# Performance work log

Hardware: AMD Instinct MI355X
Metric: run time of the kernel (lower is better)

Reference implementation:

```python
import jax, jax.numpy as jnp
import numpy as np

N_NODES = 50000
N_EDGES = 800000
LEAKY_SLOPE = 0.01
DROPOUT_P = 0.5


def _graph_conv(src, dst, x, W, b):
    """DGL GraphConv with norm='both': D_out^{-1/2} A D_in^{-1/2} X W + b."""
    n = x.shape[0]
    ones = jnp.ones((src.shape[0],), dtype=x.dtype)
    deg_out = jax.ops.segment_sum(ones, src, num_segments=n)  # out-degree of src nodes
    deg_in = jax.ops.segment_sum(ones, dst, num_segments=n)   # in-degree of dst nodes
    norm_src = jax.lax.rsqrt(jnp.maximum(deg_out, 1.0))
    norm_dst = jax.lax.rsqrt(jnp.maximum(deg_in, 1.0))
    h = (x * norm_src[:, None]) @ W          # apply weight before aggregation
    agg = jax.ops.segment_sum(h[src], dst, num_segments=n)  # SpMM aggregate
    return agg * norm_dst[:, None] + b


def _dropout(x, key, p=DROPOUT_P):
    keep = jax.random.bernoulli(key, 1.0 - p, x.shape)
    return jnp.where(keep, x / (1.0 - p), jnp.zeros((), x.dtype))


def setup_inputs() -> dict:
    key = jax.random.key(0)
    ks = jax.random.split(key, 8)
    features = jax.random.normal(ks[0], (N_NODES, 128), dtype=jnp.float32)
    src = jax.random.randint(ks[1], (N_EDGES,), 0, N_NODES, dtype=jnp.int64)
    dst = jax.random.randint(ks[2], (N_EDGES,), 0, N_NODES, dtype=jnp.int64)
    s1 = 1.0 / np.sqrt(128.0)
    s3 = 1.0 / np.sqrt(128.0)
    W1 = jax.random.normal(ks[3], (128, 128), dtype=jnp.float32) * s1
    W2 = jax.random.normal(ks[4], (128, 128), dtype=jnp.float32) * s1
    W3 = jax.random.normal(ks[5], (128, 64), dtype=jnp.float32) * s3
    b1 = jnp.zeros((128,), dtype=jnp.float32)
    b2 = jnp.zeros((128,), dtype=jnp.float32)
    b3 = jnp.zeros((64,), dtype=jnp.float32)
    return {"features": features, "src": src, "dst": dst,
            "W1": W1, "b1": b1, "W2": W2, "b2": b2, "W3": W3, "b3": b3}


def reference(features, src, dst, W1, b1, W2, b2, W3, b3):
    dk = jax.random.split(jax.random.key(42), 3)
    h = jax.nn.leaky_relu(_graph_conv(src, dst, features, W1, b1), LEAKY_SLOPE)
    h = _dropout(h, dk[0])
    h = jax.nn.leaky_relu(_graph_conv(src, dst, h, W2, b2), LEAKY_SLOPE)
    h = _dropout(h, dk[1])
    h = jax.nn.leaky_relu(_graph_conv(src, dst, h, W3, b3), LEAKY_SLOPE)
    h = _dropout(h, dk[2])
    return h
```

## Files before the change

### kernel.cpp

```cpp
#include <hip/hip_runtime.h>
#include <hip/hip_fp16.h>
#include <stdint.h>

using half8 = __attribute__((ext_vector_type(8))) _Float16;
using f32x4 = __attribute__((ext_vector_type(4))) float;

#define SLOT_CAP 64
#define LDW 136
#define NBINS 50176
#define LWORDS 12544
#define NCHUNK 128

#define TFR(r) { x0 += x1; x1 = (x1 << r) | (x1 >> (32 - r)); x1 ^= x0; }

__host__ __device__ inline void threefry2x32(uint32_t k0, uint32_t k1,
                                             uint32_t c0, uint32_t c1,
                                             uint32_t& o0, uint32_t& o1) {
  uint32_t ks2 = k0 ^ k1 ^ 0x1BD11BDAu;
  uint32_t x0 = c0 + k0, x1 = c1 + k1;
  TFR(13) TFR(15) TFR(26) TFR(6)  x0 += k1;  x1 += ks2 + 1u;
  TFR(17) TFR(29) TFR(16) TFR(24) x0 += ks2; x1 += k0 + 2u;
  TFR(13) TFR(15) TFR(26) TFR(6)  x0 += k0;  x1 += k1 + 3u;
  TFR(17) TFR(29) TFR(16) TFR(24) x0 += k1;  x1 += ks2 + 4u;
  TFR(13) TFR(15) TFR(26) TFR(6)  x0 += ks2; x1 += k0 + 5u;
  o0 = x0; o1 = x1;
}

__device__ inline float tf_uniform(uint32_t k0, uint32_t k1, uint32_t i) {
  uint32_t o0, o1;
  threefry2x32(k0, k1, 0u, i, o0, o1);
  uint32_t bits = o0 ^ o1;
  return __uint_as_float((bits >> 9) | 0x3F800000u) - 1.0f;
}

__device__ __host__ inline uint16_t f2h_bits_host(float f) {
  _Float16 h = (_Float16)f;
  union { _Float16 h; uint16_t u; } c; c.h = h; return c.u;
}
__device__ inline uint16_t f2h(float f) {
  union { _Float16 h; uint16_t u; } c; c.h = (_Float16)f; return c.u;
}
__device__ inline uint32_t pack2h(float a, float b) {
  return (uint32_t)f2h(a) | ((uint32_t)f2h(b) << 16);
}
__device__ inline __half2 u2h2(uint32_t u) {
  union { uint32_t u; __half2 h; } c; c.u = u; return c.h;
}

__device__ inline void hacc(__half2* a, uint4 r) {
  a[0] = __hadd2(a[0], u2h2(r.x));
  a[1] = __hadd2(a[1], u2h2(r.y));
  a[2] = __hadd2(a[2], u2h2(r.z));
  a[3] = __hadd2(a[3], u2h2(r.w));
}

__global__ __launch_bounds__(256) void build_hist_kernel(
    const int* __restrict__ src, const int* __restrict__ dst,
    uint16_t* __restrict__ histD, uint16_t* __restrict__ histS,
    const float* __restrict__ W1, const float* __restrict__ W2,
    const float* __restrict__ W3, uint16_t* __restrict__ Wt,
    int n, int nE, int HR, int EPB) {
  const int bid = (int)blockIdx.x;
  if (bid >= 512) {
    int i = (bid - 512) * 256 + (int)threadIdx.x;
    float v;
    if (i < 16384) {
      int nr = i >> 7, k = i & 127;
      v = W1[k * 128 + nr];
    } else if (i < 32768) {
      int j = i - 16384, nr = j >> 7, k = j & 127;
      v = W2[k * 128 + nr];
    } else if (i < 40960) {
      int j = i - 32768, nr = j >> 7, k = j & 127;
      v = W3[k * 64 + nr];
    } else return;
    Wt[i] = f2h(v);
    return;
  }

  __shared__ uint32_t bins[LWORDS];
  const bool isSrc = bid >= 256;
  const int c = bid & 127;
  const int h = (bid >> 7) & 1;
  const int lo = h * HR;
  const int* keys = isSrc ? src : dst;
  uint16_t* hist = isSrc ? histS : histD;

  for (int i = threadIdx.x; i < LWORDS; i += 256) bins[i] = 0u;
  __syncthreads();

  const int e0 = c * EPB, e1 = min(e0 + EPB, nE);
  for (int e = e0 + (int)threadIdx.x; e < e1; e += 256) {
    int k = keys[e] - lo;
    if ((unsigned)k < (unsigned)HR)
      atomicAdd(&bins[k >> 1], 1u << ((k & 1) * 16));
  }
  __syncthreads();

  uint32_t* out = (uint32_t*)(hist + (size_t)c * NBINS + lo);
  const int wlim = (min(HR, n - lo) + 1) >> 1;
  for (int i = threadIdx.x; i < wlim; i += 256) out[i] = bins[i];
}

__global__ __launch_bounds__(256) void reduce_kernel(
    uint16_t* __restrict__ histD, const uint16_t* __restrict__ histS,
    int* __restrict__ degin, float* __restrict__ nsrc, int n) {
  const int v = blockIdx.x * 256 + (int)threadIdx.x;
  if (v >= n) return;
  uint32_t run = 0;
  #pragma unroll 4
  for (int c = 0; c < NCHUNK; ++c) {
    size_t idx = (size_t)c * NBINS + v;
    uint16_t x = histD[idx];
    histD[idx] = (uint16_t)run;
    run += x;
  }
  degin[v] = (int)run;
  uint32_t s = 0;
  #pragma unroll 4
  for (int c = 0; c < NCHUNK; ++c) s += histS[(size_t)c * NBINS + v];
  nsrc[v] = rsqrtf(fmaxf((float)s, 1.0f));
}

__global__ __launch_bounds__(256) void scatter_gemm1_kernel(
    const int* __restrict__ src, const int* __restrict__ dst,
    const uint16_t* __restrict__ cumD, uint16_t* __restrict__ edge_slots,
    const float* __restrict__ X, const float* __restrict__ nsrc,
    const uint16_t* __restrict__ Wt1, uint16_t* __restrict__ h1,
    int n, int nE, int HR, int EPB) {
  __shared__ uint32_t bins[LWORDS];
  const int bid = (int)blockIdx.x;

  if (bid < 256) {
    const int c = bid & 127;
    const int h = (bid >> 7) & 1;
    const int lo = h * HR;

    for (int i = threadIdx.x; i < LWORDS; i += 256) bins[i] = 0u;
    __syncthreads();

    const int e0 = c * EPB, e1 = min(e0 + EPB, nE);
    for (int e = e0 + (int)threadIdx.x; e < e1; e += 256) {
      int d = dst[e];
      int k = d - lo;
      if ((unsigned)k < (unsigned)HR) {
        uint32_t old = atomicAdd(&bins[k >> 1], 1u << ((k & 1) * 16));
        int rank = (int)((old >> ((k & 1) * 16)) & 0xFFFFu);
        int pos = (int)cumD[(size_t)c * NBINS + d] + rank;
        if (pos < SLOT_CAP) edge_slots[((size_t)d << 6) + pos] = (uint16_t)src[e];
      }
    }
    return;
  }

  const int r0 = (bid - 256) * 64;
  const int tid = (int)threadIdx.x;
  const int wave = tid >> 6, lane = tid & 63;
  const int wm = wave & 1, wn = wave >> 1;
  const int lane15 = lane & 15, quad = lane >> 4;

  const int rowA0 = r0 + wm * 32 + lane15;
  const int rowA1 = rowA0 + 16;
  const bool v0 = rowA0 < n, v1 = rowA1 < n;

  f32x4 acc[2][4] = {};
  #pragma unroll
  for (int kc = 0; kc < 128; kc += 32) {
    const int ko = kc + quad * 8;
    half8 a0 = {}, a1 = {};
    if (v0) {
      float4 x0 = *(const float4*)&X[(size_t)rowA0 * 128 + ko];
      float4 x1 = *(const float4*)&X[(size_t)rowA0 * 128 + ko + 4];
      a0[0] = (_Float16)x0.x; a0[1] = (_Float16)x0.y;
      a0[2] = (_Float16)x0.z; a0[3] = (_Float16)x0.w;
      a0[4] = (_Float16)x1.x; a0[5] = (_Float16)x1.y;
      a0[6] = (_Float16)x1.z; a0[7] = (_Float16)x1.w;
    }
    if (v1) {
      float4 x0 = *(const float4*)&X[(size_t)rowA1 * 128 + ko];
      float4 x1 = *(const float4*)&X[(size_t)rowA1 * 128 + ko + 4];
      a1[0] = (_Float16)x0.x; a1[1] = (_Float16)x0.y;
      a1[2] = (_Float16)x0.z; a1[3] = (_Float16)x0.w;
      a1[4] = (_Float16)x1.x; a1[5] = (_Float16)x1.y;
      a1[6] = (_Float16)x1.z; a1[7] = (_Float16)x1.w;
    }
    #pragma unroll
    for (int nt = 0; nt < 4; ++nt) {
      int nn = wn * 64 + nt * 16 + lane15;
      half8 b = *(const half8*)&Wt1[nn * 128 + ko];
      acc[0][nt] = __builtin_amdgcn_mfma_f32_16x16x32_f16(a0, b, acc[0][nt], 0, 0, 0);
      acc[1][nt] = __builtin_amdgcn_mfma_f32_16x16x32_f16(a1, b, acc[1][nt], 0, 0, 0);
    }
  }

  #pragma unroll
  for (int mt = 0; mt < 2; ++mt) {
    #pragma unroll
    for (int reg = 0; reg < 4; ++reg) {
      int row = r0 + wm * 32 + mt * 16 + quad * 4 + reg;
      if (row < n) {
        float nsr = nsrc[row];
        #pragma unroll
        for (int nt = 0; nt < 4; ++nt) {
          int col = wn * 64 + nt * 16 + lane15;
          h1[(size_t)row * 128 + col] = f2h(acc[mt][nt][reg] * nsr);
        }
      }
    }
  }
}

template<int NCOLS>
__global__ __launch_bounds__(256) void fuse_gather_gemm_kernel(
    const uint16_t* __restrict__ h_in, const int* __restrict__ degin,
    const uint16_t* __restrict__ edge_slots, const float* __restrict__ nsrc,
    const float* __restrict__ bias, const uint16_t* __restrict__ Wt,
    uint16_t* __restrict__ h_out, uint32_t k0, uint32_t k1, int n) {
  __shared__ uint16_t Xs[32 * LDW];
  __shared__ float ns_s[32];
  const int r0 = (int)blockIdx.x * 32;
  const int tid = (int)threadIdx.x;

  if (tid < 32) {
    int row = r0 + tid;
    ns_s[tid] = (row < n) ? nsrc[row] : 1.0f;
  }

  const int nl = tid >> 3;
  const int node = r0 + nl;
  const int c16 = (tid & 7) * 16;

  if (node < n) {
    __half2 ha[8];
    #pragma unroll
    for (int j = 0; j < 8; ++j) ha[j] = __half2(__float2half(0.f), __float2half(0.f));

    const int dgi = degin[node];
    const int deg = min(dgi, SLOT_CAP);
    const uint16_t* slots = edge_slots + ((size_t)node << 6);
    const uint16_t* hb = h_in + c16;

    int e = 0;
    for (; e + 8 <= deg; e += 8) {
      uint4 sl = *(const uint4*)&slots[e];
      const uint16_t* p0 = hb + ((size_t)(sl.x & 0xFFFF) << 7);
      const uint16_t* p1 = hb + ((size_t)(sl.x >> 16) << 7);
      const uint16_t* p2 = hb + ((size_t)(sl.y & 0xFFFF) << 7);
      const uint16_t* p3 = hb + ((size_t)(sl.y >> 16) << 7);
      const uint16_t* p4 = hb + ((size_t)(sl.z & 0xFFFF) << 7);
      const uint16_t* p5 = hb + ((size_t)(sl.z >> 16) << 7);
      const uint16_t* p6 = hb + ((size_t)(sl.w & 0xFFFF) << 7);
      const uint16_t* p7 = hb + ((size_t)(sl.w >> 16) << 7);
      uint4 a0 = *(const uint4*)p0, b0 = *(const uint4*)(p0 + 8);
      uint4 a1 = *(const uint4*)p1, b1 = *(const uint4*)(p1 + 8);
      uint4 a2 = *(const uint4*)p2, b2 = *(const uint4*)(p2 + 8);
      uint4 a3 = *(const uint4*)p3, b3 = *(const uint4*)(p3 + 8);
      uint4 a4 = *(const uint4*)p4, b4 = *(const uint4*)(p4 + 8);
      uint4 a5 = *(const uint4*)p5, b5 = *(const uint4*)(p5 + 8);
      uint4 a6 = *(const uint4*)p6, b6 = *(const uint4*)(p6 + 8);
      uint4 a7 = *(const uint4*)p7, b7 = *(const uint4*)(p7 + 8);
      hacc(ha, a0); hacc(ha + 4, b0); hacc(ha, a1); hacc(ha + 4, b1);
      hacc(ha, a2); hacc(ha + 4, b2); hacc(ha, a3); hacc(ha + 4, b3);
      hacc(ha, a4); hacc(ha + 4, b4); hacc(ha, a5); hacc(ha + 4, b5);
      hacc(ha, a6); hacc(ha + 4, b6); hacc(ha, a7); hacc(ha + 4, b7);
    }
    for (; e < deg; ++e) {
      const uint16_t* pr = hb + ((size_t)slots[e] << 7);
      uint4 ra = *(const uint4*)pr, rb = *(const uint4*)(pr + 8);
      hacc(ha, ra); hacc(ha + 4, rb);
    }

    float acc[16];
    #pragma unroll
    for (int j = 0; j < 8; ++j) {
      float2 f = __half22float2(ha[j]);
      acc[2 * j] = f.x; acc[2 * j + 1] = f.y;
    }

    const float nd = rsqrtf(fmaxf((float)dgi, 1.0f));
    const float4 b0 = *(const float4*)&bias[c16];
    const float4 b1 = *(const float4*)&bias[c16 + 4];
    const float4 b2 = *(const float4*)&bias[c16 + 8];
    const float4 b3 = *(const float4*)&bias[c16 + 12];
    const float bb[16] = {b0.x, b0.y, b0.z, b0.w, b1.x, b1.y, b1.z, b1.w,
                          b2.x, b2.y, b2.z, b2.w, b3.x, b3.y, b3.z, b3.w};
    const uint32_t i0 = (uint32_t)(node * 128 + c16);

    float o[16];
    #pragma unroll
    for (int j = 0; j < 16; ++j) {
      float v = acc[j] * nd + bb[j];
      v = (v >= 0.f) ? v : 0.01f * v;
      o[j] = (tf_uniform(k0, k1, i0 + (uint32_t)j) < 0.5f) ? v * 2.0f : 0.0f;
    }

    uint4 w0, w1;
    w0.x = pack2h(o[0], o[1]);   w0.y = pack2h(o[2], o[3]);
    w0.z = pack2h(o[4], o[5]);   w0.w = pack2h(o[6], o[7]);
    w1.x = pack2h(o[8], o[9]);   w1.y = pack2h(o[10], o[11]);
    w1.z = pack2h(o[12], o[13]); w1.w = pack2h(o[14], o[15]);
    *(uint4*)&Xs[nl * LDW + c16] = w0;
    *(uint4*)&Xs[nl * LDW + c16 + 8] = w1;
  } else {
    uint4 z = make_uint4(0u, 0u, 0u, 0u);
    *(uint4*)&Xs[nl * LDW + c16] = z;
    *(uint4*)&Xs[nl * LDW + c16 + 8] = z;
  }
  __syncthreads();

  const int wave = tid >> 6, lane = tid & 63;
  const int wm = wave & 1, wn = wave >> 1;
  const int lane15 = lane & 15, quad = lane >> 4;
  constexpr int NT = NCOLS / 32;

  f32x4 acc[NT] = {};
  #pragma unroll
  for (int kc = 0; kc < 128; kc += 32) {
    const int ko = kc + quad * 8;
    half8 a = *(const half8*)&Xs[(wm * 16 + lane15) * LDW + ko];
    #pragma unroll
    for (int nt = 0; nt < NT; ++nt) {
      int nn = wn * (NCOLS / 2) + nt * 16 + lane15;
      half8 b = *(const half8*)&Wt[nn * 128 + ko];
      acc[nt] = __builtin_amdgcn_mfma_f32_16x16x32_f16(a, b, acc[nt], 0, 0, 0);
    }
  }

  #pragma unroll
  for (int nt = 0; nt < NT; ++nt) {
    #pragma unroll
    for (int reg = 0; reg < 4; ++reg) {
      int rl = wm * 16 + quad * 4 + reg;
      int row = r0 + rl;
      if (row < n) {
        int col = wn * (NCOLS / 2) + nt * 16 + lane15;
        h_out[(size_t)row * NCOLS + col] = f2h(acc[nt][reg] * ns_s[rl]);
      }
    }
  }
}

__global__ __launch_bounds__(256) void gather_out_kernel(
    const uint16_t* __restrict__ h3, const int* __restrict__ degin,
    const uint16_t* __restrict__ edge_slots, const float* __restrict__ bias,
    float* __restrict__ out, uint32_t k0, uint32_t k1, int n) {
  const int node = (int)blockIdx.x * 32 + (int)(threadIdx.x >> 3);
  if (node >= n) return;
  const int c8 = (threadIdx.x & 7) * 8;

  const int dgi = degin[node];
  const int deg = min(dgi, SLOT_CAP);
  const uint16_t* slots = edge_slots + ((size_t)node << 6);
  const uint16_t* hb = h3 + c8;

  __half2 ha[4];
  #pragma unroll
  for (int j = 0; j < 4; ++j) ha[j] = __half2(__float2half(0.f), __float2half(0.f));

  int e = 0;
  for (; e + 8 <= deg; e += 8) {
    uint4 sl = *(const uint4*)&slots[e];
    uint4 r0 = *(const uint4*)(hb + ((size_t)(sl.x & 0xFFFF) << 6));
    uint4 r1 = *(const uint4*)(hb + ((size_t)(sl.x >> 16) << 6));
    uint4 r2 = *(const uint4*)(hb + ((size_t)(sl.y & 0xFFFF) << 6));
    uint4 r3 = *(const uint4*)(hb + ((size_t)(sl.y >> 16) << 6));
    uint4 r4 = *(const uint4*)(hb + ((size_t)(sl.z & 0xFFFF) << 6));
    uint4 r5 = *(const uint4*)(hb + ((size_t)(sl.z >> 16) << 6));
    uint4 r6 = *(const uint4*)(hb + ((size_t)(sl.w & 0xFFFF) << 6));
    uint4 r7 = *(const uint4*)(hb + ((size_t)(sl.w >> 16) << 6));
    hacc(ha, r0); hacc(ha, r1); hacc(ha, r2); hacc(ha, r3);
    hacc(ha, r4); hacc(ha, r5); hacc(ha, r6); hacc(ha, r7);
  }
  for (; e < deg; ++e) {
    uint4 r = *(const uint4*)(hb + ((size_t)slots[e] << 6));
    hacc(ha, r);
  }

  float acc[8];
  #pragma unroll
  for (int j = 0; j < 4; ++j) {
    float2 f = __half22float2(ha[j]);
    acc[2 * j] = f.x; acc[2 * j + 1] = f.y;
  }

  const float nd = rsqrtf(fmaxf((float)dgi, 1.0f));
  const float4 b0 = *(const float4*)&bias[c8];
  const float4 b1 = *(const float4*)&bias[c8 + 4];
  const float bb[8] = {b0.x, b0.y, b0.z, b0.w, b1.x, b1.y, b1.z, b1.w};
  const uint32_t i0 = (uint32_t)(node * 64 + c8);

  float o[8];
  #pragma unroll
  for (int j = 0; j < 8; ++j) {
    float v = acc[j] * nd + bb[j];
    v = (v >= 0.f) ? v : 0.01f * v;
    o[j] = (tf_uniform(k0, k1, i0 + (uint32_t)j) < 0.5f) ? v * 2.0f : 0.0f;
  }

  float* op = &out[(size_t)node * 64 + c8];
  *(float4*)op = make_float4(o[0], o[1], o[2], o[3]);
  *(float4*)(op + 4) = make_float4(o[4], o[5], o[6], o[7]);
}

extern "C" void kernel_launch(void* const* d_in, const int* in_sizes, int n_in,
                              void* d_out, int out_size, void* d_ws, size_t ws_size,
                              hipStream_t stream) {
  const float* features = (const float*)d_in[0];
  const int*   src      = (const int*)d_in[1];
  const int*   dst      = (const int*)d_in[2];
  const float* W1       = (const float*)d_in[3];
  const float* b1       = (const float*)d_in[4];
  const float* W2       = (const float*)d_in[5];
  const float* b2       = (const float*)d_in[6];
  const float* W3       = (const float*)d_in[7];
  const float* b3       = (const float*)d_in[8];
  float* out = (float*)d_out;

  const int n  = in_sizes[0] / 128;
  const int nE = in_sizes[1];

  char* p = (char*)d_ws;
  uint16_t* histD      = (uint16_t*)p; p += (size_t)NCHUNK * NBINS * 2;
  uint16_t* histS      = (uint16_t*)p; p += (size_t)NCHUNK * NBINS * 2;
  int* degin           = (int*)p;      p += (size_t)n * 4;
  float* nsrc          = (float*)p;    p += (size_t)n * 4;
  uint16_t* edge_slots = (uint16_t*)p; p += (size_t)n * SLOT_CAP * 2;
  uint16_t* Wt         = (uint16_t*)p; p += 40960 * 2;
  uint16_t* h1         = (uint16_t*)p; p += (size_t)n * 128 * 2;
  uint16_t* h2         = (uint16_t*)p; p += (size_t)n * 128 * 2;
  uint16_t* h3         = (uint16_t*)p;

  uint32_t dk[3][2];
  for (uint32_t i = 0; i < 3; ++i)
    threefry2x32(0u, 42u, 0u, i, dk[i][0], dk[i][1]);

  const int EPB = (nE + NCHUNK - 1) / NCHUNK;
  int HR = ((n + 3) / 2) & ~1;
  if (HR > 2 * LWORDS) HR = 2 * LWORDS;
  const int gb64 = (n + 63) / 64;
  const int gb32 = (n + 31) / 32;

  build_hist_kernel<<<672, 256, 0, stream>>>(src, dst, histD, histS,
                                             W1, W2, W3, Wt, n, nE, HR, EPB);
  reduce_kernel<<<(n + 255) / 256, 256, 0, stream>>>(histD, histS, degin, nsrc, n);
  scatter_gemm1_kernel<<<256 + gb64, 256, 0, stream>>>(
      src, dst, histD, edge_slots, features, nsrc, Wt, h1, n, nE, HR, EPB);
  fuse_gather_gemm_kernel<128><<<gb32, 256, 0, stream>>>(
      h1, degin, edge_slots, nsrc, b1, Wt + 16384, h2, dk[0][0], dk[0][1], n);
  fuse_gather_gemm_kernel<64><<<gb32, 256, 0, stream>>>(
      h2, degin, edge_slots, nsrc, b2, Wt + 32768, h3, dk[1][0], dk[1][1], n);
  gather_out_kernel<<<(n + 31) / 32, 256, 0, stream>>>(
      h3, degin, edge_slots, b3, out, dk[2][0], dk[2][1], n);
}
```

Baseline: 262.6 us.

## Software-pipeline neighbor gathers with padded slot lists pointing to a zero row

After: 248.7 us. -5.3%, faster.

```diff
diff --git a/kernel.cpp b/kernel.cpp
--- a/kernel.cpp
+++ b/kernel.cpp
@@ -33,10 +33,6 @@
   return __uint_as_float((bits >> 9) | 0x3F800000u) - 1.0f;
 }
 
-__device__ __host__ inline uint16_t f2h_bits_host(float f) {
-  _Float16 h = (_Float16)f;
-  union { _Float16 h; uint16_t u; } c; c.h = h; return c.u;
-}
 __device__ inline uint16_t f2h(float f) {
   union { _Float16 h; uint16_t u; } c; c.h = (_Float16)f; return c.u;
 }
@@ -54,13 +50,79 @@
   a[3] = __hadd2(a[3], u2h2(r.w));
 }
 
+#define GDECL \
+  uint4 A0, A1, A2, A3, A4, A5, A6, A7, B0, B1, B2, B3, B4, B5, B6, B7, \
+        C0, C1, C2, C3, C4, C5, C6, C7, D0, D1, D2, D3, D4, D5, D6, D7;
+
+#define GPTRS(sl, P) \
+  const uint16_t* P##0 = hb + ((size_t)((sl).x & 0xFFFFu) << 7); \
+  const uint16_t* P##1 = hb + ((size_t)((sl).x >> 16) << 7);     \
+  const uint16_t* P##2 = hb + ((size_t)((sl).y & 0xFFFFu) << 7); \
+  const uint16_t* P##3 = hb + ((size_t)((sl).y >> 16) << 7);     \
+  const uint16_t* P##4 = hb + ((size_t)((sl).z & 0xFFFFu) << 7); \
+  const uint16_t* P##5 = hb + ((size_t)((sl).z >> 16) << 7);     \
+  const uint16_t* P##6 = hb + ((size_t)((sl).w & 0xFFFFu) << 7); \
+  const uint16_t* P##7 = hb + ((size_t)((sl).w >> 16) << 7);
+
+#define GLOAD(P, X, Y) \
+  X##0 = *(const uint4*)P##0; Y##0 = *(const uint4*)(P##0 + 8); \
+  X##1 = *(const uint4*)P##1; Y##1 = *(const uint4*)(P##1 + 8); \
+  X##2 = *(const uint4*)P##2; Y##2 = *(const uint4*)(P##2 + 8); \
+  X##3 = *(const uint4*)P##3; Y##3 = *(const uint4*)(P##3 + 8); \
+  X##4 = *(const uint4*)P##4; Y##4 = *(const uint4*)(P##4 + 8); \
+  X##5 = *(const uint4*)P##5; Y##5 = *(const uint4*)(P##5 + 8); \
+  X##6 = *(const uint4*)P##6; Y##6 = *(const uint4*)(P##6 + 8); \
+  X##7 = *(const uint4*)P##7; Y##7 = *(const uint4*)(P##7 + 8);
+
+#define GHACC(X, Y) \
+  hacc(ha, X##0); hacc(ha + 4, Y##0); \
+  hacc(ha, X##1); hacc(ha + 4, Y##1); \
+  hacc(ha, X##2); hacc(ha + 4, Y##2); \
+  hacc(ha, X##3); hacc(ha + 4, Y##3); \
+  hacc(ha, X##4); hacc(ha + 4, Y##4); \
+  hacc(ha, X##5); hacc(ha + 4, Y##5); \
+  hacc(ha, X##6); hacc(ha + 4, Y##6); \
+  hacc(ha, X##7); hacc(ha + 4, Y##7);
+
+#define ODECL uint4 A0, A1, A2, A3, A4, A5, A6, A7, C0, C1, C2, C3, C4, C5, C6, C7;
+
+#define OPTRS(sl, P) \
+  const uint16_t* P##0 = hb + ((size_t)((sl).x & 0xFFFFu) << 6); \
+  const uint16_t* P##1 = hb + ((size_t)((sl).x >> 16) << 6);     \
+  const uint16_t* P##2 = hb + ((size_t)((sl).y & 0xFFFFu) << 6); \
+  const uint16_t* P##3 = hb + ((size_t)((sl).y >> 16) << 6);     \
+  const uint16_t* P##4 = hb + ((size_t)((sl).z & 0xFFFFu) << 6); \
+  const uint16_t* P##5 = hb + ((size_t)((sl).z >> 16) << 6);     \
+  const uint16_t* P##6 = hb + ((size_t)((sl).w & 0xFFFFu) << 6); \
+  const uint16_t* P##7 = hb + ((size_t)((sl).w >> 16) << 6);
+
+#define OLOAD(P, X) \
+  X##0 = *(const uint4*)P##0; X##1 = *(const uint4*)P##1; \
+  X##2 = *(const uint4*)P##2; X##3 = *(const uint4*)P##3; \
+  X##4 = *(const uint4*)P##4; X##5 = *(const uint4*)P##5; \
+  X##6 = *(const uint4*)P##6; X##7 = *(const uint4*)P##7;
+
+#define OHACC(X) \
+  hacc(ha, X##0); hacc(ha, X##1); hacc(ha, X##2); hacc(ha, X##3); \
+  hacc(ha, X##4); hacc(ha, X##5); hacc(ha, X##6); hacc(ha, X##7);
+
 __global__ __launch_bounds__(256) void build_hist_kernel(
     const int* __restrict__ src, const int* __restrict__ dst,
     uint16_t* __restrict__ histD, uint16_t* __restrict__ histS,
     const float* __restrict__ W1, const float* __restrict__ W2,
     const float* __restrict__ W3, uint16_t* __restrict__ Wt,
+    uint16_t* __restrict__ edge_slots,
     int n, int nE, int HR, int EPB) {
   const int bid = (int)blockIdx.x;
+  if (bid >= 672) {
+    const uint32_t pk = ((uint32_t)n << 16) | (uint32_t)(n & 0xFFFF);
+    uint4 f; f.x = pk; f.y = pk; f.z = pk; f.w = pk;
+    uint4* es4 = (uint4*)edge_slots;
+    const int total = n * (SLOT_CAP / 8);
+    for (int i = (bid - 672) * 256 + (int)threadIdx.x; i < total; i += 256 * 256)
+      es4[i] = f;
+    return;
+  }
   if (bid >= 512) {
     int i = (bid - 512) * 256 + (int)threadIdx.x;
     float v;
@@ -198,20 +260,18 @@
     #pragma unroll
     for (int reg = 0; reg < 4; ++reg) {
       int row = r0 + wm * 32 + mt * 16 + quad * 4 + reg;
-      if (row < n) {
-        float nsr = nsrc[row];
-        #pragma unroll
-        for (int nt = 0; nt < 4; ++nt) {
-          int col = wn * 64 + nt * 16 + lane15;
-          h1[(size_t)row * 128 + col] = f2h(acc[mt][nt][reg] * nsr);
-        }
+      float nsr = (row < n) ? nsrc[row] : 0.0f;
+      #pragma unroll
+      for (int nt = 0; nt < 4; ++nt) {
+        int col = wn * 64 + nt * 16 + lane15;
+        h1[(size_t)row * 128 + col] = f2h(acc[mt][nt][reg] * nsr);
       }
     }
   }
 }
 
 template<int NCOLS>
-__global__ __launch_bounds__(256) void fuse_gather_gemm_kernel(
+__global__ __launch_bounds__(256, 3) void fuse_gather_gemm_kernel(
     const uint16_t* __restrict__ h_in, const int* __restrict__ degin,
     const uint16_t* __restrict__ edge_slots, const float* __restrict__ nsrc,
     const float* __restrict__ bias, const uint16_t* __restrict__ Wt,
@@ -239,35 +299,33 @@
     const int deg = min(dgi, SLOT_CAP);
     const uint16_t* slots = edge_slots + ((size_t)node << 6);
     const uint16_t* hb = h_in + c16;
-
-    int e = 0;
-    for (; e + 8 <= deg; e += 8) {
-      uint4 sl = *(const uint4*)&slots[e];
-      const uint16_t* p0 = hb + ((size_t)(sl.x & 0xFFFF) << 7);
-      const uint16_t* p1 = hb + ((size_t)(sl.x >> 16) << 7);
-      const uint16_t* p2 = hb + ((size_t)(sl.y & 0xFFFF) << 7);
-      const uint16_t* p3 = hb + ((size_t)(sl.y >> 16) << 7);
-      const uint16_t* p4 = hb + ((size_t)(sl.z & 0xFFFF) << 7);
-      const uint16_t* p5 = hb + ((size_t)(sl.z >> 16) << 7);
-      const uint16_t* p6 = hb + ((size_t)(sl.w & 0xFFFF) << 7);
-      const uint16_t* p7 = hb + ((size_t)(sl.w >> 16) << 7);
-      uint4 a0 = *(const uint4*)p0, b0 = *(const uint4*)(p0 + 8);
-      uint4 a1 = *(const uint4*)p1, b1 = *(const uint4*)(p1 + 8);
-      uint4 a2 = *(const uint4*)p2, b2 = *(const uint4*)(p2 + 8);
-      uint4 a3 = *(const uint4*)p3, b3 = *(const uint4*)(p3 + 8);
-      uint4 a4 = *(const uint4*)p4, b4 = *(const uint4*)(p4 + 8);
-      uint4 a5 = *(const uint4*)p5, b5 = *(const uint4*)(p5 + 8);
-      uint4 a6 = *(const uint4*)p6, b6 = *(const uint4*)(p6 + 8);
-      uint4 a7 = *(const uint4*)p7, b7 = *(const uint4*)(p7 + 8);
-      hacc(ha, a0); hacc(ha + 4, b0); hacc(ha, a1); hacc(ha + 4, b1);
-      hacc(ha, a2); hacc(ha + 4, b2); hacc(ha, a3); hacc(ha + 4, b3);
-      hacc(ha, a4); hacc(ha + 4, b4); hacc(ha, a5); hacc(ha + 4, b5);
-      hacc(ha, a6); hacc(ha + 4, b6); hacc(ha, a7); hacc(ha + 4, b7);
-    }
-    for (; e < deg; ++e) {
-      const uint16_t* pr = hb + ((size_t)slots[e] << 7);
-      uint4 ra = *(const uint4*)pr, rb = *(const uint4*)(pr + 8);
-      hacc(ha, ra); hacc(ha + 4, rb);
+    const int nb = (deg + 7) >> 3;
+
+    GDECL
+    if (nb > 0) {
+      uint4 sA = *(const uint4*)&slots[0];
+      GPTRS(sA, p)
+      GLOAD(p, A, B)
+      int b = 1;
+      for (; b + 1 < nb; b += 2) {
+        uint4 sB = *(const uint4*)&slots[b * 8];
+        uint4 sC = *(const uint4*)&slots[b * 8 + 8];
+        GPTRS(sB, q)
+        GLOAD(q, C, D)
+        GHACC(A, B)
+        GPTRS(sC, r)
+        GLOAD(r, A, B)
+        GHACC(C, D)
+      }
+      if (b < nb) {
+        uint4 sB = *(const uint4*)&slots[b * 8];
+        GPTRS(sB, q)
+        GLOAD(q, C, D)
+        GHACC(A, B)
+        GHACC(C, D)
+      } else {
+        GHACC(A, B)
+      }
     }
 
     float acc[16];
@@ -332,15 +390,13 @@
     for (int reg = 0; reg < 4; ++reg) {
       int rl = wm * 16 + quad * 4 + reg;
       int row = r0 + rl;
-      if (row < n) {
-        int col = wn * (NCOLS / 2) + nt * 16 + lane15;
-        h_out[(size_t)row * NCOLS + col] = f2h(acc[nt][reg] * ns_s[rl]);
-      }
-    }
-  }
-}
-
-__global__ __launch_bounds__(256) void gather_out_kernel(
+      int col = wn * (NCOLS / 2) + nt * 16 + lane15;
+      h_out[(size_t)row * NCOLS + col] = f2h(acc[nt][reg] * ns_s[rl]);
+    }
+  }
+}
+
+__global__ __launch_bounds__(256, 4) void gather_out_kernel(
     const uint16_t* __restrict__ h3, const int* __restrict__ degin,
     const uint16_t* __restrict__ edge_slots, const float* __restrict__ bias,
     float* __restrict__ out, uint32_t k0, uint32_t k1, int n) {
@@ -352,28 +408,37 @@
   const int deg = min(dgi, SLOT_CAP);
   const uint16_t* slots = edge_slots + ((size_t)node << 6);
   const uint16_t* hb = h3 + c8;
+  const int nb = (deg + 7) >> 3;
 
   __half2 ha[4];
   #pragma unroll
   for (int j = 0; j < 4; ++j) ha[j] = __half2(__float2half(0.f), __float2half(0.f));
 
-  int e = 0;
-  for (; e + 8 <= deg; e += 8) {
-    uint4 sl = *(const uint4*)&slots[e];
-    uint4 r0 = *(const uint4*)(hb + ((size_t)(sl.x & 0xFFFF) << 6));
-    uint4 r1 = *(const uint4*)(hb + ((size_t)(sl.x >> 16) << 6));
-    uint4 r2 = *(const uint4*)(hb + ((size_t)(sl.y & 0xFFFF) << 6));
-    uint4 r3 = *(const uint4*)(hb + ((size_t)(sl.y >> 16) << 6));
-    uint4 r4 = *(const uint4*)(hb + ((size_t)(sl.z & 0xFFFF) << 6));
-    uint4 r5 = *(const uint4*)(hb + ((size_t)(sl.z >> 16) << 6));
-    uint4 r6 = *(const uint4*)(hb + ((size_t)(sl.w & 0xFFFF) << 6));
-    uint4 r7 = *(const uint4*)(hb + ((size_t)(sl.w >> 16) << 6));
-    hacc(ha, r0); hacc(ha, r1); hacc(ha, r2); hacc(ha, r3);
-    hacc(ha, r4); hacc(ha, r5); hacc(ha, r6); hacc(ha, r7);
-  }
-  for (; e < deg; ++e) {
-    uint4 r = *(const uint4*)(hb + ((size_t)slots[e] << 6));
-    hacc(ha, r);
+  ODECL
+  if (nb > 0) {
+    uint4 sA = *(const uint4*)&slots[0];
+    OPTRS(sA, p)
+    OLOAD(p, A)
+    int b = 1;
+    for (; b + 1 < nb; b += 2) {
+      uint4 sB = *(const uint4*)&slots[b * 8];
+      uint4 sC = *(const uint4*)&slots[b * 8 + 8];
+      OPTRS(sB, q)
+      OLOAD(q, C)
+      OHACC(A)
+      OPTRS(sC, r)
+      OLOAD(r, A)
+      OHACC(C)
+    }
+    if (b < nb) {
+      uint4 sB = *(const uint4*)&slots[b * 8];
+      OPTRS(sB, q)
+      OLOAD(q, C)
+      OHACC(A)
+      OHACC(C)
+    } else {
+      OHACC(A)
+    }
   }
 
   float acc[8];
@@ -418,6 +483,7 @@
 
   const int n  = in_sizes[0] / 128;
   const int nE = in_sizes[1];
+  const int nA = ((n + 63) / 64) * 64;
 
   char* p = (char*)d_ws;
   uint16_t* histD      = (uint16_t*)p; p += (size_t)NCHUNK * NBINS * 2;
@@ -426,8 +492,8 @@
   float* nsrc          = (float*)p;    p += (size_t)n * 4;
   uint16_t* edge_slots = (uint16_t*)p; p += (size_t)n * SLOT_CAP * 2;
   uint16_t* Wt         = (uint16_t*)p; p += 40960 * 2;
-  uint16_t* h1         = (uint16_t*)p; p += (size_t)n * 128 * 2;
-  uint16_t* h2         = (uint16_t*)p; p += (size_t)n * 128 * 2;
+  uint16_t* h1         = (uint16_t*)p; p += (size_t)nA * 128 * 2;
+  uint16_t* h2         = (uint16_t*)p; p += (size_t)nA * 128 * 2;
   uint16_t* h3         = (uint16_t*)p;
 
   uint32_t dk[3][2];
@@ -440,8 +506,9 @@
   const int gb64 = (n + 63) / 64;
   const int gb32 = (n + 31) / 32;
 
-  build_hist_kernel<<<672, 256, 0, stream>>>(src, dst, histD, histS,
-                                             W1, W2, W3, Wt, n, nE, HR, EPB);
+  build_hist_kernel<<<928, 256, 0, stream>>>(src, dst, histD, histS,
+                                             W1, W2, W3, Wt, edge_slots,
+                                             n, nE, HR, EPB);
   reduce_kernel<<<(n + 255) / 256, 256, 0, stream>>>(histD, histS, degin, nsrc, n);
   scatter_gemm1_kernel<<<256 + gb64, 256, 0, stream>>>(
       src, dst, histD, edge_slots, features, nsrc, Wt, h1, n, nE, HR, EPB);
```

## Restructure SpMM gather to wave-per-node with padded slots and prefetching

Applied to the files above, without the earlier changes.

After: 263.2 us. No clear change (+0.3%).

```diff
diff --git a/kernel.cpp b/kernel.cpp
--- a/kernel.cpp
+++ b/kernel.cpp
@@ -33,10 +33,6 @@
   return __uint_as_float((bits >> 9) | 0x3F800000u) - 1.0f;
 }
 
-__device__ __host__ inline uint16_t f2h_bits_host(float f) {
-  _Float16 h = (_Float16)f;
-  union { _Float16 h; uint16_t u; } c; c.h = h; return c.u;
-}
 __device__ inline uint16_t f2h(float f) {
   union { _Float16 h; uint16_t u; } c; c.h = (_Float16)f; return c.u;
 }
@@ -47,20 +43,46 @@
   union { uint32_t u; __half2 h; } c; c.u = u; return c.h;
 }
 
-__device__ inline void hacc(__half2* a, uint4 r) {
-  a[0] = __hadd2(a[0], u2h2(r.x));
-  a[1] = __hadd2(a[1], u2h2(r.y));
-  a[2] = __hadd2(a[2], u2h2(r.z));
-  a[3] = __hadd2(a[3], u2h2(r.w));
-}
+#define LDF(s) (*(const uint32_t*)(h8 + (((uint32_t)(s)) << 8) + laneB))
+#define LDO(s) (*(const uint32_t*)(h8 + (((uint32_t)(s)) << 7) + laneB))
+
+#define ISSUE16(V, sa, sb, LDX) { \
+  V[0]  = LDX((sa).x & 0xFFFFu); V[1]  = LDX((sa).x >> 16); \
+  V[2]  = LDX((sa).y & 0xFFFFu); V[3]  = LDX((sa).y >> 16); \
+  V[4]  = LDX((sa).z & 0xFFFFu); V[5]  = LDX((sa).z >> 16); \
+  V[6]  = LDX((sa).w & 0xFFFFu); V[7]  = LDX((sa).w >> 16); \
+  V[8]  = LDX((sb).x & 0xFFFFu); V[9]  = LDX((sb).x >> 16); \
+  V[10] = LDX((sb).y & 0xFFFFu); V[11] = LDX((sb).y >> 16); \
+  V[12] = LDX((sb).z & 0xFFFFu); V[13] = LDX((sb).z >> 16); \
+  V[14] = LDX((sb).w & 0xFFFFu); V[15] = LDX((sb).w >> 16); }
+
+#define CONS16(V) { \
+  acc = __hadd2(acc, u2h2(V[0]));  acc = __hadd2(acc, u2h2(V[1]));  \
+  acc = __hadd2(acc, u2h2(V[2]));  acc = __hadd2(acc, u2h2(V[3]));  \
+  acc = __hadd2(acc, u2h2(V[4]));  acc = __hadd2(acc, u2h2(V[5]));  \
+  acc = __hadd2(acc, u2h2(V[6]));  acc = __hadd2(acc, u2h2(V[7]));  \
+  acc = __hadd2(acc, u2h2(V[8]));  acc = __hadd2(acc, u2h2(V[9]));  \
+  acc = __hadd2(acc, u2h2(V[10])); acc = __hadd2(acc, u2h2(V[11])); \
+  acc = __hadd2(acc, u2h2(V[12])); acc = __hadd2(acc, u2h2(V[13])); \
+  acc = __hadd2(acc, u2h2(V[14])); acc = __hadd2(acc, u2h2(V[15])); }
 
 __global__ __launch_bounds__(256) void build_hist_kernel(
     const int* __restrict__ src, const int* __restrict__ dst,
     uint16_t* __restrict__ histD, uint16_t* __restrict__ histS,
     const float* __restrict__ W1, const float* __restrict__ W2,
     const float* __restrict__ W3, uint16_t* __restrict__ Wt,
+    uint16_t* __restrict__ edge_slots,
     int n, int nE, int HR, int EPB) {
   const int bid = (int)blockIdx.x;
+  if (bid >= 672) {
+    const uint32_t pk = ((uint32_t)n << 16) | (uint32_t)(n & 0xFFFF);
+    uint4 f; f.x = pk; f.y = pk; f.z = pk; f.w = pk;
+    uint4* es4 = (uint4*)edge_slots;
+    const int total = n * (SLOT_CAP / 8);
+    for (int i = (bid - 672) * 256 + (int)threadIdx.x; i < total; i += 256 * 256)
+      es4[i] = f;
+    return;
+  }
   if (bid >= 512) {
     int i = (bid - 512) * 256 + (int)threadIdx.x;
     float v;
@@ -198,20 +220,18 @@
     #pragma unroll
     for (int reg = 0; reg < 4; ++reg) {
       int row = r0 + wm * 32 + mt * 16 + quad * 4 + reg;
-      if (row < n) {
-        float nsr = nsrc[row];
-        #pragma unroll
-        for (int nt = 0; nt < 4; ++nt) {
-          int col = wn * 64 + nt * 16 + lane15;
-          h1[(size_t)row * 128 + col] = f2h(acc[mt][nt][reg] * nsr);
-        }
+      float nsr = (row < n) ? nsrc[row] : 0.0f;
+      #pragma unroll
+      for (int nt = 0; nt < 4; ++nt) {
+        int col = wn * 64 + nt * 16 + lane15;
+        h1[(size_t)row * 128 + col] = f2h(acc[mt][nt][reg] * nsr);
       }
     }
   }
 }
 
 template<int NCOLS>
-__global__ __launch_bounds__(256) void fuse_gather_gemm_kernel(
+__global__ __launch_bounds__(256, 3) void fuse_gather_gemm_kernel(
     const uint16_t* __restrict__ h_in, const int* __restrict__ degin,
     const uint16_t* __restrict__ edge_slots, const float* __restrict__ nsrc,
     const float* __restrict__ bias, const uint16_t* __restrict__ Wt,
@@ -220,95 +240,81 @@
   __shared__ float ns_s[32];
   const int r0 = (int)blockIdx.x * 32;
   const int tid = (int)threadIdx.x;
+  const int wave = tid >> 6, lane = tid & 63;
 
   if (tid < 32) {
     int row = r0 + tid;
     ns_s[tid] = (row < n) ? nsrc[row] : 1.0f;
   }
 
-  const int nl = tid >> 3;
-  const int node = r0 + nl;
-  const int c16 = (tid & 7) * 16;
-
-  if (node < n) {
-    __half2 ha[8];
-    #pragma unroll
-    for (int j = 0; j < 8; ++j) ha[j] = __half2(__float2half(0.f), __float2half(0.f));
-
-    const int dgi = degin[node];
-    const int deg = min(dgi, SLOT_CAP);
-    const uint16_t* slots = edge_slots + ((size_t)node << 6);
-    const uint16_t* hb = h_in + c16;
-
-    int e = 0;
-    for (; e + 8 <= deg; e += 8) {
-      uint4 sl = *(const uint4*)&slots[e];
-      const uint16_t* p0 = hb + ((size_t)(sl.x & 0xFFFF) << 7);
-      const uint16_t* p1 = hb + ((size_t)(sl.x >> 16) << 7);
-      const uint16_t* p2 = hb + ((size_t)(sl.y & 0xFFFF) << 7);
-      const uint16_t* p3 = hb + ((size_t)(sl.y >> 16) << 7);
-      const uint16_t* p4 = hb + ((size_t)(sl.z & 0xFFFF) << 7);
-      const uint16_t* p5 = hb + ((size_t)(sl.z >> 16) << 7);
-      const uint16_t* p6 = hb + ((size_t)(sl.w & 0xFFFF) << 7);
-      const uint16_t* p7 = hb + ((size_t)(sl.w >> 16) << 7);
-      uint4 a0 = *(const uint4*)p0, b0 = *(const uint4*)(p0 + 8);
-      uint4 a1 = *(const uint4*)p1, b1 = *(const uint4*)(p1 + 8);
-      uint4 a2 = *(const uint4*)p2, b2 = *(const uint4*)(p2 + 8);
-      uint4 a3 = *(const uint4*)p3, b3 = *(const uint4*)(p3 + 8);
-      uint4 a4 = *(const uint4*)p4, b4 = *(const uint4*)(p4 + 8);
-      uint4 a5 = *(const uint4*)p5, b5 = *(const uint4*)(p5 + 8);
-      uint4 a6 = *(const uint4*)p6, b6 = *(const uint4*)(p6 + 8);
-      uint4 a7 = *(const uint4*)p7, b7 = *(const uint4*)(p7 + 8);
-      hacc(ha, a0); hacc(ha + 4, b0); hacc(ha, a1); hacc(ha + 4, b1);
-      hacc(ha, a2); hacc(ha + 4, b2); hacc(ha, a3); hacc(ha + 4, b3);
-      hacc(ha, a4); hacc(ha + 4, b4); hacc(ha, a5); hacc(ha + 4, b5);
-      hacc(ha, a6); hacc(ha + 4, b6); hacc(ha, a7); hacc(ha + 4, b7);
-    }
-    for (; e < deg; ++e) {
-      const uint16_t* pr = hb + ((size_t)slots[e] << 7);
-      uint4 ra = *(const uint4*)pr, rb = *(const uint4*)(pr + 8);
-      hacc(ha, ra); hacc(ha + 4, rb);
-    }
-
-    float acc[16];
-    #pragma unroll
-    for (int j = 0; j < 8; ++j) {
-      float2 f = __half22float2(ha[j]);
-      acc[2 * j] = f.x; acc[2 * j + 1] = f.y;
-    }
-
-    const float nd = rsqrtf(fmaxf((float)dgi, 1.0f));
-    const float4 b0 = *(const float4*)&bias[c16];
-    const float4 b1 = *(const float4*)&bias[c16 + 4];
-    const float4 b2 = *(const float4*)&bias[c16 + 8];
-    const float4 b3 = *(const float4*)&bias[c16 + 12];
-    const float bb[16] = {b0.x, b0.y, b0.z, b0.w, b1.x, b1.y, b1.z, b1.w,
-                          b2.x, b2.y, b2.z, b2.w, b3.x, b3.y, b3.z, b3.w};
-    const uint32_t i0 = (uint32_t)(node * 128 + c16);
-
-    float o[16];
-    #pragma unroll
-    for (int j = 0; j < 16; ++j) {
-      float v = acc[j] * nd + bb[j];
-      v = (v >= 0.f) ? v : 0.01f * v;
-      o[j] = (tf_uniform(k0, k1, i0 + (uint32_t)j) < 0.5f) ? v * 2.0f : 0.0f;
-    }
-
-    uint4 w0, w1;
-    w0.x = pack2h(o[0], o[1]);   w0.y = pack2h(o[2], o[3]);
-    w0.z = pack2h(o[4], o[5]);   w0.w = pack2h(o[6], o[7]);
-    w1.x = pack2h(o[8], o[9]);   w1.y = pack2h(o[10], o[11]);
-    w1.z = pack2h(o[12], o[13]); w1.w = pack2h(o[14], o[15]);
-    *(uint4*)&Xs[nl * LDW + c16] = w0;
-    *(uint4*)&Xs[nl * LDW + c16 + 8] = w1;
-  } else {
-    uint4 z = make_uint4(0u, 0u, 0u, 0u);
-    *(uint4*)&Xs[nl * LDW + c16] = z;
-    *(uint4*)&Xs[nl * LDW + c16 + 8] = z;
+  const char* h8 = (const char*)h_in;
+  const uint32_t laneB = (uint32_t)lane * 4u;
+  const float2 bl = *(const float2*)&bias[lane * 2];
+  const int nbase = r0 + wave * 8;
+
+  {
+    const int nc0 = min(nbase, n - 1);
+    const uint4* slp = (const uint4*)(edge_slots + ((size_t)nc0 << 6));
+    uint4 sp0 = slp[0], sp1 = slp[1], sp2 = slp[2], sp3 = slp[3];
+    int dcur = degin[nc0];
+
+    for (int k = 0; k < 8; ++k) {
+      const int node = nbase + k;
+      uint32_t v0[16], v1[16], v2[16], v3[16];
+      ISSUE16(v0, sp0, sp1, LDF)
+      ISSUE16(v1, sp2, sp3, LDF)
+
+      const int ncn = min(node + 1, n - 1);
+      const uint4* sln = (const uint4*)(edge_slots + ((size_t)ncn << 6));
+      uint4 np0 = sln[0], np1 = sln[1], np2 = sln[2], np3 = sln[3];
+      int dnxt = degin[ncn];
+
+      const int deg = min(dcur, SLOT_CAP);
+      const int nb = __builtin_amdgcn_readfirstlane((deg + 15) >> 4);
+      if (nb > 2) {
+        const int ncc = min(node, n - 1);
+        const uint4* slc = (const uint4*)(edge_slots + ((size_t)ncc << 6));
+        uint4 sx0 = slc[4], sx1 = slc[5];
+        ISSUE16(v2, sx0, sx1, LDF)
+        if (nb > 3) {
+          uint4 sy0 = slc[6], sy1 = slc[7];
+          ISSUE16(v3, sy0, sy1, LDF)
+        }
+      }
+
+      __builtin_amdgcn_sched_barrier(0);
+      const uint32_t i0 = (uint32_t)(node * 128 + lane * 2);
+      const float u0 = tf_uniform(k0, k1, i0);
+      const float u1 = tf_uniform(k0, k1, i0 + 1u);
+      __builtin_amdgcn_sched_barrier(0);
+
+      __half2 acc = u2h2(0u);
+      CONS16(v0)
+      CONS16(v1)
+      if (nb > 2) {
+        CONS16(v2)
+        if (nb > 3) { CONS16(v3) }
+      }
+
+      uint32_t w = 0u;
+      if (node < n) {
+        float2 f = __half22float2(acc);
+        const float ndv = rsqrtf(fmaxf((float)dcur, 1.0f));
+        float a0 = f.x * ndv + bl.x;
+        a0 = (a0 >= 0.f) ? a0 : 0.01f * a0;
+        a0 = (u0 < 0.5f) ? a0 * 2.0f : 0.0f;
+        float a1 = f.y * ndv + bl.y;
+        a1 = (a1 >= 0.f) ? a1 : 0.01f * a1;
+        a1 = (u1 < 0.5f) ? a1 * 2.0f : 0.0f;
+        w = pack2h(a0, a1);
+      }
+      *(uint32_t*)&Xs[(wave * 8 + k) * LDW + lane * 2] = w;
+
+      sp0 = np0; sp1 = np1; sp2 = np2; sp3 = np3; dcur = dnxt;
+    }
   }
   __syncthreads();
 
-  const int wave = tid >> 6, lane = tid & 63;
   const int wm = wave & 1, wn = wave >> 1;
   const int lane15 = lane & 15, quad = lane >> 4;
   constexpr int NT = NCOLS / 32;
@@ -332,74 +338,83 @@
     for (int reg = 0; reg < 4; ++reg) {
       int rl = wm * 16 + quad * 4 + reg;
       int row = r0 + rl;
-      if (row < n) {
-        int col = wn * (NCOLS / 2) + nt * 16 + lane15;
-        h_out[(size_t)row * NCOLS + col] = f2h(acc[nt][reg] * ns_s[rl]);
-      }
-    }
-  }
-}
-
-__global__ __launch_bounds__(256) void gather_out_kernel(
+      int col = wn * (NCOLS / 2) + nt * 16 + lane15;
+      h_out[(size_t)row * NCOLS + col] = f2h(acc[nt][reg] * ns_s[rl]);
+    }
+  }
+}
+
+__global__ __launch_bounds__(256, 3) void gather_out_kernel(
     const uint16_t* __restrict__ h3, const int* __restrict__ degin,
     const uint16_t* __restrict__ edge_slots, const float* __restrict__ bias,
     float* __restrict__ out, uint32_t k0, uint32_t k1, int n) {
-  const int node = (int)blockIdx.x * 32 + (int)(threadIdx.x >> 3);
-  if (node >= n) return;
-  const int c8 = (threadIdx.x & 7) * 8;
-
-  const int dgi = degin[node];
-  const int deg = min(dgi, SLOT_CAP);
-  const uint16_t* slots = edge_slots + ((size_t)node << 6);
-  const uint16_t* hb = h3 + c8;
-
-  __half2 ha[4];
-  #pragma unroll
-  for (int j = 0; j < 4; ++j) ha[j] = __half2(__float2half(0.f), __float2half(0.f));
-
-  int e = 0;
-  for (; e + 8 <= deg; e += 8) {
-    uint4 sl = *(const uint4*)&slots[e];
-    uint4 r0 = *(const uint4*)(hb + ((size_t)(sl.x & 0xFFFF) << 6));
-    uint4 r1 = *(const uint4*)(hb + ((size_t)(sl.x >> 16) << 6));
-    uint4 r2 = *(const uint4*)(hb + ((size_t)(sl.y & 0xFFFF) << 6));
-    uint4 r3 = *(const uint4*)(hb + ((size_t)(sl.y >> 16) << 6));
-    uint4 r4 = *(const uint4*)(hb + ((size_t)(sl.z & 0xFFFF) << 6));
-    uint4 r5 = *(const uint4*)(hb + ((size_t)(sl.z >> 16) << 6));
-    uint4 r6 = *(const uint4*)(hb + ((size_t)(sl.w & 0xFFFF) << 6));
-    uint4 r7 = *(const uint4*)(hb + ((size_t)(sl.w >> 16) << 6));
-    hacc(ha, r0); hacc(ha, r1); hacc(ha, r2); hacc(ha, r3);
-    hacc(ha, r4); hacc(ha, r5); hacc(ha, r6); hacc(ha, r7);
-  }
-  for (; e < deg; ++e) {
-    uint4 r = *(const uint4*)(hb + ((size_t)slots[e] << 6));
-    hacc(ha, r);
-  }
-
-  float acc[8];
-  #pragma unroll
-  for (int j = 0; j < 4; ++j) {
-    float2 f = __half22float2(ha[j]);
-    acc[2 * j] = f.x; acc[2 * j + 1] = f.y;
-  }
-
-  const float nd = rsqrtf(fmaxf((float)dgi, 1.0f));
-  const float4 b0 = *(const float4*)&bias[c8];
-  const float4 b1 = *(const float4*)&bias[c8 + 4];
-  const float bb[8] = {b0.x, b0.y, b0.z, b0.w, b1.x, b1.y, b1.z, b1.w};
-  const uint32_t i0 = (uint32_t)(node * 64 + c8);
-
-  float o[8];
-  #pragma unroll
-  for (int j = 0; j < 8; ++j) {
-    float v = acc[j] * nd + bb[j];
-    v = (v >= 0.f) ? v : 0.01f * v;
-    o[j] = (tf_uniform(k0, k1, i0 + (uint32_t)j) < 0.5f) ? v * 2.0f : 0.0f;
-  }
-
-  float* op = &out[(size_t)node * 64 + c8];
-  *(float4*)op = make_float4(o[0], o[1], o[2], o[3]);
-  *(float4*)(op + 4) = make_float4(o[4], o[5], o[6], o[7]);
+  const int tid = (int)threadIdx.x;
+  const int wave = tid >> 6, lane = tid & 63;
+  const int half = lane >> 5, l32 = lane & 31;
+  const int nbase = (int)blockIdx.x * 32 + wave * 8;
+  const char* h8 = (const char*)h3;
+  const uint32_t laneB = (uint32_t)l32 * 4u;
+  const float2 bl = *(const float2*)&bias[l32 * 2];
+
+  const int nc0 = min(nbase + half, n - 1);
+  const uint4* slp = (const uint4*)(edge_slots + ((size_t)nc0 << 6));
+  uint4 sp0 = slp[0], sp1 = slp[1], sp2 = slp[2], sp3 = slp[3];
+  int dcur = degin[nc0];
+
+  for (int p = 0; p < 4; ++p) {
+    const int nodep = nbase + p * 2 + half;
+    uint32_t v0[16], v1[16], v2[16], v3[16];
+    ISSUE16(v0, sp0, sp1, LDO)
+    ISSUE16(v1, sp2, sp3, LDO)
+
+    const int ncn = min(nbase + (p + 1) * 2 + half, n - 1);
+    const uint4* sln = (const uint4*)(edge_slots + ((size_t)ncn << 6));
+    uint4 np0 = sln[0], np1 = sln[1], np2 = sln[2], np3 = sln[3];
+    int dnxt = degin[ncn];
+
+    const int deg = min(dcur, SLOT_CAP);
+    int nbl = (deg + 15) >> 4;
+    int nbo = __shfl_xor(nbl, 32);
+    const int nb = __builtin_amdgcn_readfirstlane(max(nbl, nbo));
+    if (nb > 2) {
+      const int ncc = min(nodep, n - 1);
+      const uint4* slc = (const uint4*)(edge_slots + ((size_t)ncc << 6));
+      uint4 sx0 = slc[4], sx1 = slc[5];
+      ISSUE16(v2, sx0, sx1, LDO)
+      if (nb > 3) {
+        uint4 sy0 = slc[6], sy1 = slc[7];
+        ISSUE16(v3, sy0, sy1, LDO)
+      }
+    }
+
+    __builtin_amdgcn_sched_barrier(0);
+    const uint32_t i0 = (uint32_t)(nodep * 64 + l32 * 2);
+    const float u0 = tf_uniform(k0, k1, i0);
+    const float u1 = tf_uniform(k0, k1, i0 + 1u);
+    __builtin_amdgcn_sched_barrier(0);
+
+    __half2 acc = u2h2(0u);
+    CONS16(v0)
+    CONS16(v1)
+    if (nb > 2) {
+      CONS16(v2)
+      if (nb > 3) { CONS16(v3) }
+    }
+
+    if (nodep < n) {
+      float2 f = __half22float2(acc);
+      const float ndv = rsqrtf(fmaxf((float)dcur, 1.0f));
+      float a0 = f.x * ndv + bl.x;
+      a0 = (a0 >= 0.f) ? a0 : 0.01f * a0;
+      a0 = (u0 < 0.5f) ? a0 * 2.0f : 0.0f;
+      float a1 = f.y * ndv + bl.y;
+      a1 = (a1 >= 0.f) ? a1 : 0.01f * a1;
+      a1 = (u1 < 0.5f) ? a1 * 2.0f : 0.0f;
+      *(float2*)&out[(size_t)nodep * 64 + l32 * 2] = make_float2(a0, a1);
+    }
+
+    sp0 = np0; sp1 = np1; sp2 = np2; sp3 = np3; dcur = dnxt;
+  }
 }
 
 extern "C" void kernel_launch(void* const* d_in, const int* in_sizes, int n_in,
@@ -418,6 +433,7 @@
 
   const int n  = in_sizes[0] / 128;
   const int nE = in_sizes[1];
+  const int nA = ((n + 63) / 64) * 64;
 
   char* p = (char*)d_ws;
   uint16_t* histD      = (uint16_t*)p; p += (size_t)NCHUNK * NBINS * 2;
@@ -426,8 +442,8 @@
   float* nsrc          = (float*)p;    p += (size_t)n * 4;
   uint16_t* edge_slots = (uint16_t*)p; p += (size_t)n * SLOT_CAP * 2;
   uint16_t* Wt         = (uint16_t*)p; p += 40960 * 2;
-  uint16_t* h1         = (uint16_t*)p; p += (size_t)n * 128 * 2;
-  uint16_t* h2         = (uint16_t*)p; p += (size_t)n * 128 * 2;
+  uint16_t* h1         = (uint16_t*)p; p += (size_t)nA * 128 * 2;
+  uint16_t* h2         = (uint16_t*)p; p += (size_t)nA * 128 * 2;
   uint16_t* h3         = (uint16_t*)p;
 
   uint32_t dk[3][2];
@@ -440,8 +456,9 @@
   const int gb64 = (n + 63) / 64;
   const int gb32 = (n + 31) / 32;
 
-  build_hist_kernel<<<672, 256, 0, stream>>>(src, dst, histD, histS,
-                                             W1, W2, W3, Wt, n, nE, HR, EPB);
+  build_hist_kernel<<<928, 256, 0, stream>>>(src, dst, histD, histS,
+                                             W1, W2, W3, Wt, edge_slots,
+                                             n, nE, HR, EPB);
   reduce_kernel<<<(n + 255) / 256, 256, 0, stream>>>(histD, histS, degin, nsrc, n);
   scatter_gemm1_kernel<<<256 + gb64, 256, 0, stream>>>(
       src, dst, histD, edge_slots, features, nsrc, Wt, h1, n, nE, HR, EPB);
```
